# Optimization experiments

Hardware: AMD Instinct MI355X
Metric: run time of the kernel (lower is better)

## Reference

```python
import jax, jax.numpy as jnp
import numpy as np

B, S, H, F, E, K = 4, 4096, 1024, 4096, 8, 2


def setup_inputs() -> dict:
    key = jax.random.key(0)
    ks = jax.random.split(key, 4)
    x = jax.random.normal(ks[0], (B, S, H), dtype=jnp.float32)
    Wg = jax.random.normal(ks[1], (H, E), dtype=jnp.float32) * (1.0 / np.sqrt(H))
    W1 = jax.random.normal(ks[2], (E, H, F), dtype=jnp.float32) * (1.0 / np.sqrt(H))
    b1 = jnp.zeros((E, F), dtype=jnp.float32)
    W2 = jax.random.normal(ks[3], (E, F, H), dtype=jnp.float32) * (1.0 / np.sqrt(F))
    b2 = jnp.zeros((E, H), dtype=jnp.float32)
    return {"x": x, "Wg": Wg, "W1": W1, "b1": b1, "W2": W2, "b2": b2}


def reference(x, Wg, W1, b1, W2, b2):
    b, s, h = x.shape
    e = W1.shape[0]
    xf = x.reshape(-1, h)                      # [N, H]
    logits = xf @ Wg                           # [N, E] router logits
    top_vals, top_idx = jax.lax.top_k(logits, K)   # [N, K]
    gate_w = jax.nn.softmax(top_vals, axis=-1)     # softmax over selected experts
    # combine weights per expert: [N, E]
    comb = jnp.sum(gate_w[..., None] * jax.nn.one_hot(top_idx, e, dtype=xf.dtype), axis=1)
    out = jnp.zeros_like(xf)
    for ei in range(e):  # fixed small expert count
        hdd = jax.nn.gelu(xf @ W1[ei] + b1[ei])    # [N, F]
        y = hdd @ W2[ei] + b2[ei]                  # [N, H]
        out = out + comb[:, ei:ei + 1] * y
    return out.reshape(b, s, h)
```

## Files before the change

kernel.cpp:

```cpp
#include <hip/hip_runtime.h>
#include <hip/hip_bf16.h>

#define N_TOK 16384
#define HD 1024
#define FD 4096
#define NE 8

typedef __attribute__((ext_vector_type(8))) short short8;
typedef __attribute__((ext_vector_type(4))) float f32x4;

__device__ __forceinline__ unsigned short f2b(float f) {
  union { __hip_bfloat16 h; unsigned short u; } c;
  c.h = __float2bfloat16(f);
  return c.u;
}

__device__ __forceinline__ float gelu_tanh(float x) {
  const float c = 0.7978845608028654f;
  float u = c * (x + 0.044715f * x * x * x);
  float t = 1.0f - 2.0f / (__expf(2.0f * u) + 1.0f);
  return 0.5f * x * (1.0f + t);
}

__device__ __forceinline__ void gload_lds16(const void* g, void* l) {
  __builtin_amdgcn_global_load_lds((const __attribute__((address_space(1))) void*)g,
                                   (__attribute__((address_space(3))) void*)l, 16, 0, 0);
}

__global__ void cvt_x(const float* __restrict__ x, unsigned short* __restrict__ xb) {
  int i = blockIdx.x * 256 + threadIdx.x;
  float4 v = ((const float4*)x)[i];
  ushort4 u;
  u.x = f2b(v.x); u.y = f2b(v.y); u.z = f2b(v.z); u.w = f2b(v.w);
  ((ushort4*)xb)[i] = u;
}

__global__ void transpose_cvt(const float* __restrict__ in, unsigned short* __restrict__ out,
                              int R, int C) {
  __shared__ float tile[32][33];
  const size_t mo = (size_t)blockIdx.z * R * C;
  const float* ip = in + mo;
  unsigned short* op = out + mo;
  int c0 = blockIdx.x * 32, r0 = blockIdx.y * 32;
  int tx = threadIdx.x, ty = threadIdx.y;
#pragma unroll
  for (int j = 0; j < 4; j++)
    tile[ty + j * 8][tx] = ip[(size_t)(r0 + ty + j * 8) * C + (c0 + tx)];
  __syncthreads();
#pragma unroll
  for (int j = 0; j < 4; j++)
    op[(size_t)(c0 + ty + j * 8) * R + (r0 + tx)] = f2b(tile[tx][ty + j * 8]);
}

__global__ void router(const float* __restrict__ x, const float* __restrict__ wg,
                       int* __restrict__ counts, int* __restrict__ tok_idx,
                       float* __restrict__ tok_w) {
  int wid = threadIdx.x >> 6;
  int lane = threadIdx.x & 63;
  int t = blockIdx.x * 4 + wid;
  const float* xr = x + (size_t)t * HD;
  float acc[NE];
#pragma unroll
  for (int e = 0; e < NE; e++) acc[e] = 0.0f;
  for (int i = lane; i < HD; i += 64) {
    float xv = xr[i];
    const float* wr = wg + i * NE;
#pragma unroll
    for (int e = 0; e < NE; e++) acc[e] += xv * wr[e];
  }
#pragma unroll
  for (int e = 0; e < NE; e++) {
    for (int off = 32; off > 0; off >>= 1) acc[e] += __shfl_down(acc[e], off);
  }
  if (lane == 0) {
    int i0 = 0; float v0 = acc[0];
#pragma unroll
    for (int e = 1; e < NE; e++) { if (acc[e] > v0) { v0 = acc[e]; i0 = e; } }
    int i1 = -1; float v1 = -1e30f;
#pragma unroll
    for (int e = 0; e < NE; e++) { if (e != i0 && acc[e] > v1) { v1 = acc[e]; i1 = e; } }
    float w0 = 1.0f / (1.0f + __expf(v1 - v0));
    float w1 = 1.0f - w0;
    int s0 = atomicAdd(&counts[i0], 1);
    tok_idx[i0 * N_TOK + s0] = t; tok_w[i0 * N_TOK + s0] = w0;
    int s1 = atomicAdd(&counts[i1], 1);
    tok_idx[i1 * N_TOK + s1] = t; tok_w[i1 * N_TOK + s1] = w1;
  }
}

__global__ void scan_counts(const int* __restrict__ counts, int* __restrict__ offsets) {
  int s = 0;
  for (int e = 0; e < NE; e++) { offsets[e] = s; s += counts[e]; }
  offsets[NE] = s;
}

template <bool IS_G1, int KD, int ND>
__global__ __launch_bounds__(256) void moe_gemm(
    const unsigned short* __restrict__ A, const unsigned short* __restrict__ Bt,
    const float* __restrict__ bias, const int* __restrict__ counts,
    const int* __restrict__ offsets, const int* __restrict__ tok_idx,
    const float* __restrict__ tok_w, unsigned short* __restrict__ hdd,
    float* __restrict__ out) {
  const int e = blockIdx.z;
  const int cnt = counts[e];
  const int m0 = blockIdx.y * 128;
  if (m0 >= cnt) return;
  const int n0 = blockIdx.x * 128;
  const int offs = offsets[e];

  __shared__ unsigned short lA[128 * 32];
  __shared__ unsigned short lB[128 * 32];

  const int tid = threadIdx.x;
  const int r0 = tid >> 2, r1 = 64 + (tid >> 2);
  const int ck = (tid & 3) * 8;

  const unsigned short *aB0, *aB1;
  if constexpr (IS_G1) {
    const int* tl = tok_idx + e * N_TOK;
    int t0 = tl[min(m0 + r0, cnt - 1)];
    int t1 = tl[min(m0 + r1, cnt - 1)];
    aB0 = A + (size_t)t0 * KD + ck;
    aB1 = A + (size_t)t1 * KD + ck;
  } else {
    aB0 = A + (size_t)(offs + m0 + r0) * KD + ck;
    aB1 = A + (size_t)(offs + m0 + r1) * KD + ck;
  }
  const unsigned short* bBase = Bt + (size_t)e * ND * KD;
  const unsigned short* bB0 = bBase + (size_t)(n0 + r0) * KD + ck;
  const unsigned short* bB1 = bBase + (size_t)(n0 + r1) * KD + ck;

  const int lane = tid & 63;
  const int wid = tid >> 6;
  const int wm = (wid >> 1) * 64, wn = (wid & 1) * 64;
  const int lrow = lane & 15, lkg = lane >> 4;

  f32x4 acc[4][4] = {};

  for (int k0 = 0; k0 < KD; k0 += 32) {
    gload_lds16(aB0 + k0, &lA[tid * 8]);
    gload_lds16(aB1 + k0, &lA[2048 + tid * 8]);
    gload_lds16(bB0 + k0, &lB[tid * 8]);
    gload_lds16(bB1 + k0, &lB[2048 + tid * 8]);
    __syncthreads();
    short8 af[4], bf[4];
#pragma unroll
    for (int i = 0; i < 4; i++)
      af[i] = *(const short8*)&lA[(wm + i * 16 + lrow) * 32 + lkg * 8];
#pragma unroll
    for (int i = 0; i < 4; i++)
      bf[i] = *(const short8*)&lB[(wn + i * 16 + lrow) * 32 + lkg * 8];
#pragma unroll
    for (int mi = 0; mi < 4; mi++)
#pragma unroll
      for (int ni = 0; ni < 4; ni++)
        acc[mi][ni] = __builtin_amdgcn_mfma_f32_16x16x32_bf16(af[mi], bf[ni], acc[mi][ni], 0, 0, 0);
    __syncthreads();
  }

  if constexpr (IS_G1) {
#pragma unroll
    for (int mi = 0; mi < 4; mi++) {
      int mbase = m0 + wm + mi * 16 + lkg * 4;
#pragma unroll
      for (int r = 0; r < 4; r++) {
        int m = mbase + r;
        if (m < cnt) {
          __hip_bfloat16* hrow = (__hip_bfloat16*)(hdd + (size_t)(offs + m) * FD);
#pragma unroll
          for (int ni = 0; ni < 4; ni++) {
            int n = n0 + wn + ni * 16 + lrow;
            float v = acc[mi][ni][r] + bias[e * ND + n];
            hrow[n] = __float2bfloat16(gelu_tanh(v));
          }
        }
      }
    }
  } else {
    const int* tl = tok_idx + e * N_TOK;
    const float* wl = tok_w + e * N_TOK;
#pragma unroll
    for (int mi = 0; mi < 4; mi++) {
      int mbase = m0 + wm + mi * 16 + lkg * 4;
#pragma unroll
      for (int r = 0; r < 4; r++) {
        int m = mbase + r;
        if (m < cnt) {
          int t = tl[m];
          float w = wl[m];
          float* orow = out + (size_t)t * HD;
#pragma unroll
          for (int ni = 0; ni < 4; ni++) {
            int n = n0 + wn + ni * 16 + lrow;
            float v = acc[mi][ni][r] + bias[e * ND + n];
            atomicAdd(&orow[n], w * v);
          }
        }
      }
    }
  }
}

extern "C" void kernel_launch(void* const* d_in, const int* in_sizes, int n_in,
                              void* d_out, int out_size, void* d_ws, size_t ws_size,
                              hipStream_t stream) {
  const float* x  = (const float*)d_in[0];
  const float* Wg = (const float*)d_in[1];
  const float* W1 = (const float*)d_in[2];
  const float* b1 = (const float*)d_in[3];
  const float* W2 = (const float*)d_in[4];
  const float* b2 = (const float*)d_in[5];
  float* out = (float*)d_out;

  char* ws = (char*)d_ws;
  int* counts       = (int*)(ws + 0);
  int* offsets      = (int*)(ws + 64);
  int* tok_idx      = (int*)(ws + 256);
  float* tok_w      = (float*)(ws + 524544);
  unsigned short* xb  = (unsigned short*)(ws + 1048832);
  unsigned short* w1t = (unsigned short*)(ws + 34603264);
  unsigned short* w2t = (unsigned short*)(ws + 101712128);
  unsigned short* hdd = (unsigned short*)(ws + 168820992);

  hipMemsetAsync(counts, 0, 64, stream);
  hipMemsetAsync(d_out, 0, (size_t)N_TOK * HD * sizeof(float), stream);

  cvt_x<<<(N_TOK * HD / 4) / 256, 256, 0, stream>>>(x, xb);
  transpose_cvt<<<dim3(FD / 32, HD / 32, NE), dim3(32, 8), 0, stream>>>(W1, w1t, HD, FD);
  transpose_cvt<<<dim3(HD / 32, FD / 32, NE), dim3(32, 8), 0, stream>>>(W2, w2t, FD, HD);
  router<<<N_TOK / 4, 256, 0, stream>>>(x, Wg, counts, tok_idx, tok_w);
  scan_counts<<<1, 1, 0, stream>>>(counts, offsets);

  moe_gemm<true, HD, FD><<<dim3(FD / 128, N_TOK / 128, NE), 256, 0, stream>>>(
      xb, w1t, b1, counts, offsets, tok_idx, tok_w, hdd, out);
  moe_gemm<false, FD, HD><<<dim3(HD / 128, N_TOK / 128, NE), 256, 0, stream>>>(
      hdd, w2t, b2, counts, offsets, tok_idx, tok_w, hdd, out);
}
```

Before: 1.688 ms.

## Swizzle LDS tiles and replace atomic scatter with bf16 buffer plus combine kernel

Applies an XOR swizzle to the k-chunk column used when loading A/B tiles into LDS and when reading MFMA fragments, to reduce LDS bank conflicts. The second GEMM now writes per-slot bf16 expert outputs into a buffer that reuses the dead W1 workspace. A new combine kernel gathers each token's two expert rows and weights them into the output, removing fp32 atomicAdds and the output memset. This adds an extra pass over the buffer and rounds expert outputs to bf16 before combining.

```diff
diff --git a/kernel.cpp b/kernel.cpp
--- a/kernel.cpp
+++ b/kernel.cpp
@@ -13,6 +13,12 @@
   union { __hip_bfloat16 h; unsigned short u; } c;
   c.h = __float2bfloat16(f);
   return c.u;
+}
+
+__device__ __forceinline__ float b2f(unsigned short u) {
+  union { float f; unsigned int i; } c;
+  c.i = ((unsigned int)u) << 16;
+  return c.f;
 }
 
 __device__ __forceinline__ float gelu_tanh(float x) {
@@ -54,7 +60,8 @@
 
 __global__ void router(const float* __restrict__ x, const float* __restrict__ wg,
                        int* __restrict__ counts, int* __restrict__ tok_idx,
-                       float* __restrict__ tok_w) {
+                       float* __restrict__ tok_w, int* __restrict__ inv_es,
+                       float* __restrict__ inv_w) {
   int wid = threadIdx.x >> 6;
   int lane = threadIdx.x & 63;
   int t = blockIdx.x * 4 + wid;
@@ -85,6 +92,8 @@
     tok_idx[i0 * N_TOK + s0] = t; tok_w[i0 * N_TOK + s0] = w0;
     int s1 = atomicAdd(&counts[i1], 1);
     tok_idx[i1 * N_TOK + s1] = t; tok_w[i1 * N_TOK + s1] = w1;
+    inv_es[2 * t + 0] = (i0 << 16) | s0;  inv_w[2 * t + 0] = w0;
+    inv_es[2 * t + 1] = (i1 << 16) | s1;  inv_w[2 * t + 1] = w1;
   }
 }
 
@@ -99,8 +108,7 @@
     const unsigned short* __restrict__ A, const unsigned short* __restrict__ Bt,
     const float* __restrict__ bias, const int* __restrict__ counts,
     const int* __restrict__ offsets, const int* __restrict__ tok_idx,
-    const float* __restrict__ tok_w, unsigned short* __restrict__ hdd,
-    float* __restrict__ out) {
+    unsigned short* __restrict__ hdd, unsigned short* __restrict__ y) {
   const int e = blockIdx.z;
   const int cnt = counts[e];
   const int m0 = blockIdx.y * 128;
@@ -113,27 +121,28 @@
 
   const int tid = threadIdx.x;
   const int r0 = tid >> 2, r1 = 64 + (tid >> 2);
-  const int ck = (tid & 3) * 8;
+  const int cks = (((tid & 3) ^ ((tid >> 3) & 3))) * 8;
 
   const unsigned short *aB0, *aB1;
   if constexpr (IS_G1) {
     const int* tl = tok_idx + e * N_TOK;
     int t0 = tl[min(m0 + r0, cnt - 1)];
     int t1 = tl[min(m0 + r1, cnt - 1)];
-    aB0 = A + (size_t)t0 * KD + ck;
-    aB1 = A + (size_t)t1 * KD + ck;
+    aB0 = A + (size_t)t0 * KD + cks;
+    aB1 = A + (size_t)t1 * KD + cks;
   } else {
-    aB0 = A + (size_t)(offs + m0 + r0) * KD + ck;
-    aB1 = A + (size_t)(offs + m0 + r1) * KD + ck;
+    aB0 = A + (size_t)(offs + m0 + r0) * KD + cks;
+    aB1 = A + (size_t)(offs + m0 + r1) * KD + cks;
   }
   const unsigned short* bBase = Bt + (size_t)e * ND * KD;
-  const unsigned short* bB0 = bBase + (size_t)(n0 + r0) * KD + ck;
-  const unsigned short* bB1 = bBase + (size_t)(n0 + r1) * KD + ck;
+  const unsigned short* bB0 = bBase + (size_t)(n0 + r0) * KD + cks;
+  const unsigned short* bB1 = bBase + (size_t)(n0 + r1) * KD + cks;
 
   const int lane = tid & 63;
   const int wid = tid >> 6;
   const int wm = (wid >> 1) * 64, wn = (wid & 1) * 64;
   const int lrow = lane & 15, lkg = lane >> 4;
+  const int rdk = (lkg ^ ((lrow >> 1) & 3)) * 8;
 
   f32x4 acc[4][4] = {};
 
@@ -146,10 +155,10 @@
     short8 af[4], bf[4];
 #pragma unroll
     for (int i = 0; i < 4; i++)
-      af[i] = *(const short8*)&lA[(wm + i * 16 + lrow) * 32 + lkg * 8];
+      af[i] = *(const short8*)&lA[(wm + i * 16 + lrow) * 32 + rdk];
 #pragma unroll
     for (int i = 0; i < 4; i++)
-      bf[i] = *(const short8*)&lB[(wn + i * 16 + lrow) * 32 + lkg * 8];
+      bf[i] = *(const short8*)&lB[(wn + i * 16 + lrow) * 32 + rdk];
 #pragma unroll
     for (int mi = 0; mi < 4; mi++)
 #pragma unroll
@@ -158,14 +167,14 @@
     __syncthreads();
   }
 
-  if constexpr (IS_G1) {
-#pragma unroll
-    for (int mi = 0; mi < 4; mi++) {
-      int mbase = m0 + wm + mi * 16 + lkg * 4;
-#pragma unroll
-      for (int r = 0; r < 4; r++) {
-        int m = mbase + r;
-        if (m < cnt) {
+#pragma unroll
+  for (int mi = 0; mi < 4; mi++) {
+    int mbase = m0 + wm + mi * 16 + lkg * 4;
+#pragma unroll
+    for (int r = 0; r < 4; r++) {
+      int m = mbase + r;
+      if (m < cnt) {
+        if constexpr (IS_G1) {
           __hip_bfloat16* hrow = (__hip_bfloat16*)(hdd + (size_t)(offs + m) * FD);
 #pragma unroll
           for (int ni = 0; ni < 4; ni++) {
@@ -173,32 +182,38 @@
             float v = acc[mi][ni][r] + bias[e * ND + n];
             hrow[n] = __float2bfloat16(gelu_tanh(v));
           }
-        }
-      }
-    }
-  } else {
-    const int* tl = tok_idx + e * N_TOK;
-    const float* wl = tok_w + e * N_TOK;
-#pragma unroll
-    for (int mi = 0; mi < 4; mi++) {
-      int mbase = m0 + wm + mi * 16 + lkg * 4;
-#pragma unroll
-      for (int r = 0; r < 4; r++) {
-        int m = mbase + r;
-        if (m < cnt) {
-          int t = tl[m];
-          float w = wl[m];
-          float* orow = out + (size_t)t * HD;
+        } else {
+          __hip_bfloat16* yrow = (__hip_bfloat16*)(y + (size_t)(offs + m) * HD);
 #pragma unroll
           for (int ni = 0; ni < 4; ni++) {
             int n = n0 + wn + ni * 16 + lrow;
             float v = acc[mi][ni][r] + bias[e * ND + n];
-            atomicAdd(&orow[n], w * v);
+            yrow[n] = __float2bfloat16(v);
           }
         }
       }
     }
   }
+}
+
+__global__ void combine(const unsigned short* __restrict__ y, const int* __restrict__ offsets,
+                        const int* __restrict__ inv_es, const float* __restrict__ inv_w,
+                        float* __restrict__ out) {
+  int t = blockIdx.x;
+  int p0 = inv_es[2 * t], p1 = inv_es[2 * t + 1];
+  float w0 = inv_w[2 * t], w1 = inv_w[2 * t + 1];
+  int g0 = offsets[p0 >> 16] + (p0 & 0xffff);
+  int g1 = offsets[p1 >> 16] + (p1 & 0xffff);
+  const ushort4* ra = (const ushort4*)(y + (size_t)g0 * HD);
+  const ushort4* rb = (const ushort4*)(y + (size_t)g1 * HD);
+  int i = threadIdx.x;
+  ushort4 a = ra[i], b = rb[i];
+  float4 o;
+  o.x = w0 * b2f(a.x) + w1 * b2f(b.x);
+  o.y = w0 * b2f(a.y) + w1 * b2f(b.y);
+  o.z = w0 * b2f(a.z) + w1 * b2f(b.z);
+  o.w = w0 * b2f(a.w) + w1 * b2f(b.w);
+  ((float4*)(out + (size_t)t * HD))[i] = o;
 }
 
 extern "C" void kernel_launch(void* const* d_in, const int* in_sizes, int n_in,
@@ -217,22 +232,25 @@
   int* offsets      = (int*)(ws + 64);
   int* tok_idx      = (int*)(ws + 256);
   float* tok_w      = (float*)(ws + 524544);
-  unsigned short* xb  = (unsigned short*)(ws + 1048832);
-  unsigned short* w1t = (unsigned short*)(ws + 34603264);
-  unsigned short* w2t = (unsigned short*)(ws + 101712128);
-  unsigned short* hdd = (unsigned short*)(ws + 168820992);
+  int* inv_es       = (int*)(ws + 1048832);
+  float* inv_w      = (float*)(ws + 1179904);
+  unsigned short* xb  = (unsigned short*)(ws + 1310976);
+  unsigned short* w1t = (unsigned short*)(ws + 34865408);
+  unsigned short* yb  = (unsigned short*)(ws + 34865408);
+  unsigned short* w2t = (unsigned short*)(ws + 101974272);
+  unsigned short* hdd = (unsigned short*)(ws + 169083136);
 
   hipMemsetAsync(counts, 0, 64, stream);
-  hipMemsetAsync(d_out, 0, (size_t)N_TOK * HD * sizeof(float), stream);
 
   cvt_x<<<(N_TOK * HD / 4) / 256, 256, 0, stream>>>(x, xb);
   transpose_cvt<<<dim3(FD / 32, HD / 32, NE), dim3(32, 8), 0, stream>>>(W1, w1t, HD, FD);
   transpose_cvt<<<dim3(HD / 32, FD / 32, NE), dim3(32, 8), 0, stream>>>(W2, w2t, FD, HD);
-  router<<<N_TOK / 4, 256, 0, stream>>>(x, Wg, counts, tok_idx, tok_w);
+  router<<<N_TOK / 4, 256, 0, stream>>>(x, Wg, counts, tok_idx, tok_w, inv_es, inv_w);
   scan_counts<<<1, 1, 0, stream>>>(counts, offsets);
 
   moe_gemm<true, HD, FD><<<dim3(FD / 128, N_TOK / 128, NE), 256, 0, stream>>>(
-      xb, w1t, b1, counts, offsets, tok_idx, tok_w, hdd, out);
+      xb, w1t, b1, counts, offsets, tok_idx, hdd, yb);
   moe_gemm<false, FD, HD><<<dim3(HD / 128, N_TOK / 128, NE), 256, 0, stream>>>(
-      hdd, w2t, b2, counts, offsets, tok_idx, tok_w, hdd, out);
-}
+      hdd, w2t, b2, counts, offsets, tok_idx, hdd, yb);
+  combine<<<N_TOK, 256, 0, stream>>>(yb, offsets, inv_es, inv_w, out);
+}
```

Result: faster. 1.583 ms (-6.2%).
